# Kernel optimization log

Measured on AMD Instinct MI355X. Metric: run time of the kernel, lower is better.

## Reference

```python
import jax, jax.numpy as jnp
import numpy as np

B, S, V, E, H = 512, 512, 128, 128, 256


def setup_inputs() -> dict:
    key = jax.random.key(0)
    ks = jax.random.split(key, 12)
    s_e = 1.0 / np.sqrt(E)
    s_h = 1.0 / np.sqrt(H)
    inp = {
        "x": jax.random.randint(ks[0], (B, S), 0, V, dtype=jnp.int64),
        "emb": jax.random.normal(ks[1], (V, E), dtype=jnp.float32) * 0.02,
        # layer 0: input dim E
        "Wi0": jax.random.uniform(ks[2], (4 * H, E), jnp.float32, -s_e, s_e),
        "bi0": jax.random.uniform(ks[3], (4 * H,), jnp.float32, -s_e, s_e),
        "Wh0": jax.random.uniform(ks[4], (4 * H, H), jnp.float32, -s_h, s_h),
        "bh0": jax.random.uniform(ks[5], (4 * H,), jnp.float32, -s_h, s_h),
        # layer 1: input dim H
        "Wi1": jax.random.uniform(ks[6], (4 * H, H), jnp.float32, -s_h, s_h),
        "bi1": jax.random.uniform(ks[7], (4 * H,), jnp.float32, -s_h, s_h),
        "Wh1": jax.random.uniform(ks[8], (4 * H, H), jnp.float32, -s_h, s_h),
        "bh1": jax.random.uniform(ks[9], (4 * H,), jnp.float32, -s_h, s_h),
        # fc_gen: hidden -> vocab
        "Wg": jax.random.uniform(ks[10], (V, H), jnp.float32, -s_h, s_h),
        "bg": jax.random.uniform(ks[11], (V,), jnp.float32, -s_h, s_h),
    }
    return inp


def lstm_layer(x_seq, Wi, bi, Wh, bh):
    """x_seq: [B,S,D] -> hidden states [B,S,H]. Gate order f,i,g,o (chunk order)."""
    b, s, _ = x_seq.shape
    h_dim = Wh.shape[1]
    # precompute input contribution for all timesteps in one big matmul
    xg = jnp.einsum("bsd,gd->bsg", x_seq, Wi) + bi  # [B,S,4H]

    def step(carry, xg_t):
        h, c = carry
        gates = xg_t + h @ Wh.T + bh  # [B,4H]
        f, i, g, o = jnp.split(gates, 4, axis=-1)
        c = jax.nn.sigmoid(f) * c + jax.nn.sigmoid(i) * jnp.tanh(g)
        h = jax.nn.sigmoid(o) * jnp.tanh(c)
        return (h, c), h

    init = (jnp.zeros((b, h_dim), x_seq.dtype), jnp.zeros((b, h_dim), x_seq.dtype))
    _, hs = jax.lax.scan(step, init, jnp.swapaxes(xg, 0, 1))  # hs: [S,B,H]
    return jnp.swapaxes(hs, 0, 1)


def reference(x, emb, Wi0, bi0, Wh0, bh0, Wi1, bi1, Wh1, bh1, Wg, bg):
    # Embedding lookup
    e = emb[x]  # [B,S,E]
    # Forward-direction stacked LSTM (backward direction never affects logits;
    # dropout is identity at inference)
    h1 = lstm_layer(e, Wi0, bi0, Wh0, bh0)   # [B,S,H]
    h2 = lstm_layer(h1, Wi1, bi1, Wh1, bh1)  # [B,S,H]
    logits = h2 @ Wg.T + bg                  # [B,S,V]
    return logits
```

## Files before the change

kernel.cpp:

```cpp
#include <hip/hip_runtime.h>
#include <hip/hip_bf16.h>

#define BB 512
#define SS 512
#define EE 128
#define HH 256
#define VV 128
#define G4H 1024
#define TSL 64
#define NSEG (SS / TSL)

using bf16 = __bf16;
typedef __attribute__((ext_vector_type(8))) __bf16 bf16x8;
typedef __attribute__((ext_vector_type(4))) float f32x4;

__device__ __forceinline__ float rcpf(float x) { return __builtin_amdgcn_rcpf(x); }
__device__ __forceinline__ float exp2f_(float x) { return __builtin_amdgcn_exp2f(x); }
__device__ __forceinline__ float sigf(float x) {
  return rcpf(1.0f + exp2f_(-1.442695041f * x));
}
__device__ __forceinline__ float tanh_(float x) {
  return 2.0f * rcpf(1.0f + exp2f_(-2.885390082f * x)) - 1.0f;
}
__device__ __forceinline__ bf16x8 cvt8(const float* __restrict__ s) {
  bf16x8 f;
  #pragma unroll
  for (int j = 0; j < 8; ++j) f[j] = (bf16)s[j];
  return f;
}
__device__ __forceinline__ float bf2f(unsigned short u) {
  return __uint_as_float(((unsigned)u) << 16);
}

__global__ void detect_kernel(const int* __restrict__ x, int* __restrict__ flag) {
  const int i = blockIdx.x * 256 + threadIdx.x;
  if (x[2 * i + 1] != 0) atomicOr(flag, 1);
}

__global__ __launch_bounds__(256)
void table_kernel(const float* __restrict__ emb, const float* __restrict__ Wi,
                  const float* __restrict__ bi, const float* __restrict__ bh,
                  unsigned short* __restrict__ table) {
  const int g = blockIdx.x * 256 + threadIdx.x;
  const int v = blockIdx.y;
  float s = bi[g] + bh[g];
  const float* er = emb + v * EE;
  const float* wr = Wi + (size_t)g * EE;
  #pragma unroll 4
  for (int e = 0; e < EE; ++e) s += er[e] * wr[e];
  const bf16 b = (bf16)s;
  table[v * G4H + (g & 255) * 4 + (g >> 8)] = *(const unsigned short*)&b;
}

__global__ __launch_bounds__(256)
void wprep_kernel(const float* __restrict__ Wh0, const float* __restrict__ Wh1,
                  bf16x8* __restrict__ wb0, bf16x8* __restrict__ wb1) {
  const int idx = blockIdx.x * 256 + threadIdx.x;
  const int l = idx & 63, kc = (idx >> 6) & 7, s = (idx >> 9) & 7, w = idx >> 12;
  const int lg = l >> 4, ln = l & 15;
  const int n = (s >> 1) * HH + w * 32 + 16 * (s & 1) + ln;
  const int k0 = kc * 32 + lg * 8;
  const float* src = (blockIdx.y ? Wh1 : Wh0) + (size_t)n * HH + k0;
  (blockIdx.y ? wb1 : wb0)[idx] = cvt8(src);
}

__device__ __forceinline__
void rec0_body(char* smem, const int* __restrict__ x, int is32,
               const bf16x8* __restrict__ wb,
               const unsigned short* __restrict__ table,
               bf16* __restrict__ h1, float (*cst)[4],
               int t0, int bid, bool load_h) {
  bf16 (*hbuf)[4096] = (bf16(*)[4096])smem;
  bf16x8* wlds = (bf16x8*)(smem + 16384);
  const int tid = threadIdx.x, w = tid >> 6, l = tid & 63, lg = l >> 4, ln = l & 15;
  const int b0 = bid * 16, hb = w * 32;

  bf16x8 Wf[4][8];
  #pragma unroll
  for (int s = 0; s < 4; ++s)
    #pragma unroll
    for (int kc = 0; kc < 8; ++kc)
      Wf[s][kc] = wb[w * 4096 + s * 512 + kc * 64 + l];
  #pragma unroll
  for (int j = 0; j < 2; ++j)
    #pragma unroll
    for (int kc = 0; kc < 8; ++kc)
      wlds[((w * 2 + j) * 8 + kc) * 64 + l] = wb[w * 4096 + (6 + j) * 512 + kc * 64 + l];
  const bf16x8* __restrict__ gsrc0 = wb + w * 4096 + 4 * 512 + l;
  const bf16x8* __restrict__ gsrc1 = wb + w * 4096 + 5 * 512 + l;

  int hoff[4];
  #pragma unroll
  for (int r = 0; r < 4; ++r)
    hoff[r] = ((b0 + lg * 4 + r) * SS) * HH + hb + ln;

  if (t0 == 0) {
    bf16x8 z = {};
    ((bf16x8*)&hbuf[0][0])[tid] = z;
  } else if (load_h) {
    #pragma unroll
    for (int j = 0; j < 2; ++j)
      #pragma unroll
      for (int r = 0; r < 4; ++r) {
        const int m = lg * 4 + r, col = hb + 16 * j + ln;
        const bf16 hv = h1[((size_t)(b0 + m) * SS + (t0 - 1)) * HH + col];
        hbuf[0][(w * 64 + m * 4 + 2 * j + (ln >> 3)) * 8 + (ln & 7)] = hv;
      }
  }
  int idx[4];
  #pragma unroll
  for (int r = 0; r < 4; ++r) {
    const long xi = (long)(b0 + lg * 4 + r) * SS + t0;
    idx[r] = x[is32 ? xi : 2 * xi] & 127;
  }
  __syncthreads();

  #pragma unroll 1
  for (int tt = 0; tt < TSL; ++tt) {
    const int t = t0 + tt, p = tt & 1;
    ushort4 tj[4][2];
    #pragma unroll
    for (int r = 0; r < 4; ++r) {
      const unsigned short* base = table + (size_t)idx[r] * G4H + (hb + ln) * 4;
      tj[r][0] = *(const ushort4*)base;
      tj[r][1] = *(const ushort4*)(base + 64);
    }
    if (tt + 1 < TSL) {
      #pragma unroll
      for (int r = 0; r < 4; ++r) {
        const long xi = (long)(b0 + lg * 4 + r) * SS + (t + 1);
        idx[r] = x[is32 ? xi : 2 * xi] & 127;
      }
    }
    f32x4 acc[4][2] = {};
    #pragma unroll
    for (int kc = 0; kc < 8; ++kc) {
      bf16x8 a = ((const bf16x8*)&hbuf[p][0])[kc * 64 + ln * 4 + lg];
      acc[0][0] = __builtin_amdgcn_mfma_f32_16x16x32_bf16(a, Wf[0][kc], acc[0][0], 0, 0, 0);
      acc[0][1] = __builtin_amdgcn_mfma_f32_16x16x32_bf16(a, Wf[1][kc], acc[0][1], 0, 0, 0);
      acc[1][0] = __builtin_amdgcn_mfma_f32_16x16x32_bf16(a, Wf[2][kc], acc[1][0], 0, 0, 0);
      acc[1][1] = __builtin_amdgcn_mfma_f32_16x16x32_bf16(a, Wf[3][kc], acc[1][1], 0, 0, 0);
      acc[2][0] = __builtin_amdgcn_mfma_f32_16x16x32_bf16(a, gsrc0[kc * 64], acc[2][0], 0, 0, 0);
      acc[2][1] = __builtin_amdgcn_mfma_f32_16x16x32_bf16(a, gsrc1[kc * 64], acc[2][1], 0, 0, 0);
      #pragma unroll
      for (int j = 0; j < 2; ++j) {
        bf16x8 bw = wlds[((w * 2 + j) * 8 + kc) * 64 + l];
        acc[3][j] = __builtin_amdgcn_mfma_f32_16x16x32_bf16(a, bw, acc[3][j], 0, 0, 0);
      }
    }
    #pragma unroll
    for (int j = 0; j < 2; ++j)
      #pragma unroll
      for (int r = 0; r < 4; ++r) {
        const float fg = sigf(acc[0][j][r] + bf2f(tj[r][j].x));
        const float ig = sigf(acc[1][j][r] + bf2f(tj[r][j].y));
        const float gg = tanh_(acc[2][j][r] + bf2f(tj[r][j].z));
        const float og = sigf(acc[3][j][r] + bf2f(tj[r][j].w));
        const float cc = fg * cst[j][r] + ig * gg;
        cst[j][r] = cc;
        const bf16 hv = (bf16)(og * tanh_(cc));
        const int m = lg * 4 + r;
        hbuf[p ^ 1][(w * 64 + m * 4 + 2 * j + (ln >> 3)) * 8 + (ln & 7)] = hv;
        h1[hoff[r] + t * HH + 16 * j] = hv;
      }
    __syncthreads();
  }
}

__device__ __forceinline__
void rec1_body(char* smem, const unsigned short* __restrict__ xg,
               const bf16x8* __restrict__ wb, bf16* __restrict__ hreg,
               float* __restrict__ cws, int t0, int bid) {
  bf16 (*hbuf)[4096] = (bf16(*)[4096])smem;
  bf16x8* wlds = (bf16x8*)(smem + 16384);
  const int tid = threadIdx.x, w = tid >> 6, l = tid & 63, lg = l >> 4, ln = l & 15;
  const int b0 = bid * 16, hb = w * 32;

  bf16x8 Wf[4][8];
  #pragma unroll
  for (int s = 0; s < 4; ++s)
    #pragma unroll
    for (int kc = 0; kc < 8; ++kc)
      Wf[s][kc] = wb[w * 4096 + s * 512 + kc * 64 + l];
  #pragma unroll
  for (int j = 0; j < 2; ++j)
    #pragma unroll
    for (int kc = 0; kc < 8; ++kc)
      wlds[((w * 2 + j) * 8 + kc) * 64 + l] = wb[w * 4096 + (6 + j) * 512 + kc * 64 + l];
  const bf16x8* __restrict__ gsrc0 = wb + w * 4096 + 4 * 512 + l;
  const bf16x8* __restrict__ gsrc1 = wb + w * 4096 + 5 * 512 + l;

  int hoff[4];
  size_t xbase[4];
  #pragma unroll
  for (int r = 0; r < 4; ++r) {
    hoff[r] = ((b0 + lg * 4 + r) * SS) * HH + hb + ln;
    xbase[r] = (size_t)(b0 + lg * 4 + r) * TSL * G4H + (hb + ln) * 4;
  }

  float c[2][4];
  if (t0 == 0) {
    #pragma unroll
    for (int j = 0; j < 2; ++j)
      #pragma unroll
      for (int r = 0; r < 4; ++r) c[j][r] = 0.f;
    bf16x8 z = {};
    ((bf16x8*)&hbuf[0][0])[tid] = z;
  } else {
    #pragma unroll
    for (int j = 0; j < 2; ++j)
      #pragma unroll
      for (int r = 0; r < 4; ++r) {
        const int m = lg * 4 + r, col = hb + 16 * j + ln;
        c[j][r] = cws[(size_t)(b0 + m) * HH + col];
        const bf16 hv = hreg[((size_t)(b0 + m) * SS + (t0 - 1)) * HH + col];
        hbuf[0][(w * 64 + m * 4 + 2 * j + (ln >> 3)) * 8 + (ln & 7)] = hv;
      }
  }
  __syncthreads();

  #pragma unroll 1
  for (int tt = 0; tt < TSL; ++tt) {
    const int t = t0 + tt, p = tt & 1;
    ushort4 tj[4][2];
    #pragma unroll
    for (int r = 0; r < 4; ++r) {
      const unsigned short* base = xg + xbase[r] + (size_t)tt * G4H;
      tj[r][0] = *(const ushort4*)base;
      tj[r][1] = *(const ushort4*)(base + 64);
    }
    f32x4 acc[4][2] = {};
    #pragma unroll
    for (int kc = 0; kc < 8; ++kc) {
      bf16x8 a = ((const bf16x8*)&hbuf[p][0])[kc * 64 + ln * 4 + lg];
      acc[0][0] = __builtin_amdgcn_mfma_f32_16x16x32_bf16(a, Wf[0][kc], acc[0][0], 0, 0, 0);
      acc[0][1] = __builtin_amdgcn_mfma_f32_16x16x32_bf16(a, Wf[1][kc], acc[0][1], 0, 0, 0);
      acc[1][0] = __builtin_amdgcn_mfma_f32_16x16x32_bf16(a, Wf[2][kc], acc[1][0], 0, 0, 0);
      acc[1][1] = __builtin_amdgcn_mfma_f32_16x16x32_bf16(a, Wf[3][kc], acc[1][1], 0, 0, 0);
      acc[2][0] = __builtin_amdgcn_mfma_f32_16x16x32_bf16(a, gsrc0[kc * 64], acc[2][0], 0, 0, 0);
      acc[2][1] = __builtin_amdgcn_mfma_f32_16x16x32_bf16(a, gsrc1[kc * 64], acc[2][1], 0, 0, 0);
      #pragma unroll
      for (int j = 0; j < 2; ++j) {
        bf16x8 bw = wlds[((w * 2 + j) * 8 + kc) * 64 + l];
        acc[3][j] = __builtin_amdgcn_mfma_f32_16x16x32_bf16(a, bw, acc[3][j], 0, 0, 0);
      }
    }
    #pragma unroll
    for (int j = 0; j < 2; ++j)
      #pragma unroll
      for (int r = 0; r < 4; ++r) {
        const float fg = sigf(acc[0][j][r] + bf2f(tj[r][j].x));
        const float ig = sigf(acc[1][j][r] + bf2f(tj[r][j].y));
        const float gg = tanh_(acc[2][j][r] + bf2f(tj[r][j].z));
        const float og = sigf(acc[3][j][r] + bf2f(tj[r][j].w));
        const float cc = fg * c[j][r] + ig * gg;
        c[j][r] = cc;
        const bf16 hv = (bf16)(og * tanh_(cc));
        const int m = lg * 4 + r;
        hbuf[p ^ 1][(w * 64 + m * 4 + 2 * j + (ln >> 3)) * 8 + (ln & 7)] = hv;
        hreg[hoff[r] + t * HH + 16 * j] = hv;
      }
    __syncthreads();
  }
  #pragma unroll
  for (int j = 0; j < 2; ++j)
    #pragma unroll
    for (int r = 0; r < 4; ++r)
      cws[(size_t)(b0 + lg * 4 + r) * HH + hb + 16 * j + ln] = c[j][r];
}

__device__ __forceinline__
void xg_body(char* smem, const bf16* __restrict__ A, const float* __restrict__ W,
             const float* __restrict__ bias0, const float* __restrict__ bias1,
             bf16* __restrict__ out, int t0, int flat) {
  bf16x8* alds = (bf16x8*)smem;
  bf16x8* blds = (bf16x8*)(smem + 65536);
  const int tid = threadIdx.x, w = tid >> 6, l = tid & 63, lg = l >> 4, ln = l & 15;
  const int wm = w & 1, wn = w >> 1;
  const int R0 = (flat & 255) * 128, N0 = (flat >> 8) * 128;
  {
    const int row = tid >> 2, seg = tid & 3;
    const int R = R0 + row;
    const bf16* asrc = A + ((size_t)(R >> 6) * SS + t0 + (R & 63)) * HH + seg * 64;
    #pragma unroll
    for (int k = 0; k < 8; ++k) {
      const int g = seg * 8 + k;
      alds[row * 32 + (g ^ (row & 7))] = *(const bf16x8*)(asrc + k * 8);
    }
    const float* bsrc = W + (size_t)(N0 + row) * HH + seg * 64;
    #pragma unroll
    for (int k = 0; k < 8; ++k) {
      const int g = seg * 8 + k;
      blds[row * 32 + (g ^ (row & 7))] = cvt8(bsrc + k * 8);
    }
  }
  __syncthreads();
  f32x4 acc[4][2] = {};
  #pragma unroll
  for (int kc = 0; kc < 8; ++kc) {
    bf16x8 bfr[2];
    #pragma unroll
    for (int nt = 0; nt < 2; ++nt) {
      const int row = wn * 32 + nt * 16 + ln;
      bfr[nt] = blds[row * 32 + ((kc * 4 + lg) ^ (row & 7))];
    }
    #pragma unroll
    for (int mt = 0; mt < 4; ++mt) {
      const int row = wm * 64 + mt * 16 + ln;
      bf16x8 a = alds[row * 32 + ((kc * 4 + lg) ^ (row & 7))];
      #pragma unroll
      for (int nt = 0; nt < 2; ++nt)
        acc[mt][nt] = __builtin_amdgcn_mfma_f32_16x16x32_bf16(a, bfr[nt], acc[mt][nt], 0, 0, 0);
    }
  }
  #pragma unroll
  for (int nt = 0; nt < 2; ++nt) {
    const int n = N0 + wn * 32 + nt * 16 + ln;
    const float bv = bias0[n] + bias1[n];
    const int col = (n & 255) * 4 + (n >> 8);
    #pragma unroll
    for (int mt = 0; mt < 4; ++mt)
      #pragma unroll
      for (int r = 0; r < 4; ++r) {
        const size_t row = (size_t)R0 + wm * 64 + mt * 16 + lg * 4 + r;
        out[row * G4H + col] = (bf16)(acc[mt][nt][r] + bv);
      }
  }
}

__device__ __forceinline__
void rec0_slice(char* smem, const int* x, int is32, const bf16x8* wb0,
                const unsigned short* table, bf16* hreg, float* cws0,
                int t0, int bid) {
  const int tid = threadIdx.x, w = tid >> 6, l = tid & 63, lg = l >> 4, ln = l & 15;
  const int b0 = bid * 16, hb = w * 32;
  float c[2][4];
  if (t0 == 0) {
    #pragma unroll
    for (int j = 0; j < 2; ++j)
      #pragma unroll
      for (int r = 0; r < 4; ++r) c[j][r] = 0.f;
  } else {
    #pragma unroll
    for (int j = 0; j < 2; ++j)
      #pragma unroll
      for (int r = 0; r < 4; ++r)
        c[j][r] = cws0[(size_t)(b0 + lg * 4 + r) * HH + hb + 16 * j + ln];
  }
  rec0_body(smem, x, is32, wb0, table, hreg, c, t0, bid, t0 != 0);
  #pragma unroll
  for (int j = 0; j < 2; ++j)
    #pragma unroll
    for (int r = 0; r < 4; ++r)
      cws0[(size_t)(b0 + lg * 4 + r) * HH + hb + 16 * j + ln] = c[j][r];
}

__global__ __launch_bounds__(512)
void pipe_kernel(const int* __restrict__ x, const int* __restrict__ flagp,
                 const bf16x8* __restrict__ wb0,
                 const unsigned short* __restrict__ table,
                 const unsigned short* __restrict__ xg_in,
                 const bf16x8* __restrict__ wb1,
                 bf16* __restrict__ hreg, float* __restrict__ cws0,
                 float* __restrict__ cws1, int k,
                 const float* __restrict__ Wi, const float* __restrict__ bi,
                 const float* __restrict__ bh, bf16* __restrict__ xg_out) {
  __shared__ __align__(16) char smem[147456];
  const int bx = blockIdx.x;
  if (bx < 32) {
    if (k < NSEG) rec0_slice(smem, x, *flagp, wb0, table, hreg, cws0, k * TSL, bx);
  } else if (bx < 64) {
    if (k >= 2) rec1_body(smem, xg_in, wb1, hreg, cws1, (k - 2) * TSL, bx - 32);
  } else {
    if (k >= 1 && k <= NSEG)
      xg_body(smem, hreg, Wi, bi, bh, xg_out, (k - 1) * TSL, bx - 64);
  }
}

__global__ __launch_bounds__(512)
void rec0_full_kernel(const int* __restrict__ x, const int* __restrict__ flagp,
                      const bf16x8* __restrict__ wb,
                      const unsigned short* __restrict__ table,
                      bf16* __restrict__ h1) {
  __shared__ __align__(16) char smem[147456];
  const int is32 = *flagp;
  float c[2][4] = {};
  #pragma unroll 1
  for (int s = 0; s < NSEG; ++s) {
    rec0_body(smem, x, is32, wb, table, h1, c, s * TSL, blockIdx.x, false);
    __syncthreads();
  }
}

__global__ __launch_bounds__(512)
void combo_kernel(const unsigned short* __restrict__ xg_in,
                  const bf16x8* __restrict__ wb, bf16* __restrict__ hreg,
                  float* __restrict__ cws, int t0,
                  const float* __restrict__ Wi, const float* __restrict__ bi,
                  const float* __restrict__ bh, bf16* __restrict__ xg_out) {
  __shared__ __align__(16) char smem[147456];
  if (blockIdx.x < 32)
    rec1_body(smem, xg_in, wb, hreg, cws, t0, blockIdx.x);
  else
    xg_body(smem, hreg, Wi, bi, bh, xg_out, t0 + TSL, blockIdx.x - 32);
}

template <int OUT_BF16>
__global__ __launch_bounds__(512)
void gemm_kernel(const bf16* __restrict__ A, const float* __restrict__ W,
                 const float* __restrict__ bias0, const float* __restrict__ bias1,
                 void* __restrict__ out, int t0, int NCOL) {
  __shared__ bf16x8 alds[4096];
  __shared__ bf16x8 blds[4096];
  const int tid = threadIdx.x, w = tid >> 6, l = tid & 63, lg = l >> 4, ln = l & 15;
  const int wm = w & 1, wn = w >> 1;
  const int R0 = blockIdx.x * 128, N0 = blockIdx.y * 128;
  {
    const int row = tid >> 2, seg = tid & 3;
    const bf16* asrc;
    if (OUT_BF16) {
      const int R = R0 + row;
      asrc = A + ((size_t)(R >> 6) * SS + t0 + (R & 63)) * HH + seg * 64;
    } else {
      asrc = A + ((size_t)R0 + row) * HH + seg * 64;
    }
    #pragma unroll
    for (int k = 0; k < 8; ++k) {
      const int g = seg * 8 + k;
      alds[row * 32 + (g ^ (row & 7))] = *(const bf16x8*)(asrc + k * 8);
    }
    const float* bsrc = W + (size_t)(N0 + row) * HH + seg * 64;
    #pragma unroll
    for (int k = 0; k < 8; ++k) {
      const int g = seg * 8 + k;
      blds[row * 32 + (g ^ (row & 7))] = cvt8(bsrc + k * 8);
    }
  }
  __syncthreads();
  f32x4 acc[4][2] = {};
  #pragma unroll
  for (int kc = 0; kc < 8; ++kc) {
    bf16x8 bfr[2];
    #pragma unroll
    for (int nt = 0; nt < 2; ++nt) {
      const int row = wn * 32 + nt * 16 + ln;
      bfr[nt] = blds[row * 32 + ((kc * 4 + lg) ^ (row & 7))];
    }
    #pragma unroll
    for (int mt = 0; mt < 4; ++mt) {
      const int row = wm * 64 + mt * 16 + ln;
      bf16x8 a = alds[row * 32 + ((kc * 4 + lg) ^ (row & 7))];
      #pragma unroll
      for (int nt = 0; nt < 2; ++nt)
        acc[mt][nt] = __builtin_amdgcn_mfma_f32_16x16x32_bf16(a, bfr[nt], acc[mt][nt], 0, 0, 0);
    }
  }
  #pragma unroll
  for (int nt = 0; nt < 2; ++nt) {
    const int n = N0 + wn * 32 + nt * 16 + ln;
    const float bv = bias0[n] + (bias1 ? bias1[n] : 0.f);
    const int col = OUT_BF16 ? ((n & 255) * 4 + (n >> 8)) : n;
    #pragma unroll
    for (int mt = 0; mt < 4; ++mt)
      #pragma unroll
      for (int r = 0; r < 4; ++r) {
        const size_t row = (size_t)R0 + wm * 64 + mt * 16 + lg * 4 + r;
        if (OUT_BF16) ((bf16*)out)[row * NCOL + col] = (bf16)(acc[mt][nt][r] + bv);
        else          ((float*)out)[row * NCOL + col] = acc[mt][nt][r] + bv;
      }
  }
}

extern "C" void kernel_launch(void* const* d_in, const int* in_sizes, int n_in,
                              void* d_out, int out_size, void* d_ws, size_t ws_size,
                              hipStream_t stream) {
  const int*   x   = (const int*)d_in[0];
  const float* emb = (const float*)d_in[1];
  const float* Wi0 = (const float*)d_in[2];
  const float* bi0 = (const float*)d_in[3];
  const float* Wh0 = (const float*)d_in[4];
  const float* bh0 = (const float*)d_in[5];
  const float* Wi1 = (const float*)d_in[6];
  const float* bi1 = (const float*)d_in[7];
  const float* Wh1 = (const float*)d_in[8];
  const float* bh1 = (const float*)d_in[9];
  const float* Wg  = (const float*)d_in[10];
  const float* bg  = (const float*)d_in[11];

  char* ws = (char*)d_ws;
  int* flag = (int*)ws;
  unsigned short* table = (unsigned short*)(ws + 256);
  bf16x8* wb0 = (bf16x8*)(ws + 256 + 262144);
  bf16x8* wb1 = (bf16x8*)(ws + 256 + 262144 + 524288);
  bf16* hreg = (bf16*)(ws + 256 + 262144 + 524288 + 524288);
  const size_t need_base = 256 + 262144 + 524288 + 524288
                         + (size_t)BB * SS * HH * sizeof(bf16);
  float* cws0 = (float*)(ws + need_base);
  float* cws1 = (float*)(ws + need_base + 524288);
  const size_t need_full = need_base + 2 * 524288;
  if (ws_size < need_base) return;

  bf16* xgbuf0 = (bf16*)d_out;
  bf16* xgbuf1 = (bf16*)((char*)d_out + (size_t)BB * TSL * G4H * sizeof(bf16));

  (void)hipMemsetAsync(flag, 0, sizeof(int), stream);
  detect_kernel<<<dim3(8), dim3(256), 0, stream>>>(x, flag);
  table_kernel<<<dim3(4, 128), dim3(256), 0, stream>>>(emb, Wi0, bi0, bh0, table);
  wprep_kernel<<<dim3(128, 2), dim3(256), 0, stream>>>(Wh0, Wh1, wb0, wb1);

  if (ws_size >= need_full) {
    for (int k = 0; k <= NSEG + 1; ++k) {
      bf16* xin  = (k & 1) ? xgbuf1 : xgbuf0;
      bf16* xout = (k & 1) ? xgbuf0 : xgbuf1;
      const bool xgv = (k >= 1 && k <= NSEG);
      const int nblk = 64 + (xgv ? 2048 : 0);
      pipe_kernel<<<dim3(nblk), dim3(512), 0, stream>>>(
          x, flag, wb0, table, (const unsigned short*)xin, wb1,
          hreg, cws0, cws1, k, Wi1, bi1, bh1, xout);
    }
  } else {
    float* cwsA = (float*)wb0;
    rec0_full_kernel<<<dim3(32), dim3(512), 0, stream>>>(x, flag, wb0, table, hreg);
    gemm_kernel<1><<<dim3(256, 8), dim3(512), 0, stream>>>(
        hreg, Wi1, bi1, bh1, xgbuf0, 0, G4H);
    for (int s = 0; s < NSEG; ++s) {
      const int t0 = s * TSL;
      bf16* xin  = (s & 1) ? xgbuf1 : xgbuf0;
      bf16* xout = (s & 1) ? xgbuf0 : xgbuf1;
      const int nblk = 32 + ((s + 1 < NSEG) ? 2048 : 0);
      combo_kernel<<<dim3(nblk), dim3(512), 0, stream>>>(
          (const unsigned short*)xin, wb1, hreg, cwsA, t0, Wi1, bi1, bh1, xout);
    }
  }
  gemm_kernel<0><<<dim3(BB * SS / 128, VV / 128), dim3(512), 0, stream>>>(
      hreg, Wg, bg, nullptr, d_out, 0, VV);
}
```

Baseline: 2.882 ms.

## Retile layer-1 input-gate GEMM to 64x256 tiles with gate-interleaved weight columns

The xg GEMM tile changes from 128 rows x 128 columns to 64 rows (one batch row block across 64 timesteps) x 256 interleaved gate columns. Weight rows are gathered so the output columns come out contiguous in the interleaved gate layout. This is meant to give each tile contiguous row reads and coalesced, contiguous output writes. The cost is a larger B tile, so each 64-row A tile is paired with four times more weight conversion work, and LDS grows to 160KB. The generic gemm template is split into separate xg and projection kernels.

```diff
diff --git a/kernel.cpp b/kernel.cpp
--- a/kernel.cpp
+++ b/kernel.cpp
@@ -274,56 +274,59 @@
              const float* __restrict__ bias0, const float* __restrict__ bias1,
              bf16* __restrict__ out, int t0, int flat) {
   bf16x8* alds = (bf16x8*)smem;
-  bf16x8* blds = (bf16x8*)(smem + 65536);
+  bf16x8* blds = (bf16x8*)(smem + 32768);
   const int tid = threadIdx.x, w = tid >> 6, l = tid & 63, lg = l >> 4, ln = l & 15;
   const int wm = w & 1, wn = w >> 1;
-  const int R0 = (flat & 255) * 128, N0 = (flat >> 8) * 128;
+  const int rb = flat & 511, up = flat >> 9;
+  const int R0 = rb * 64;
   {
-    const int row = tid >> 2, seg = tid & 3;
-    const int R = R0 + row;
-    const bf16* asrc = A + ((size_t)(R >> 6) * SS + t0 + (R & 63)) * HH + seg * 64;
-    #pragma unroll
-    for (int k = 0; k < 8; ++k) {
-      const int g = seg * 8 + k;
+    const int row = tid >> 3, seg = tid & 7;
+    const bf16* asrc = A + ((size_t)rb * SS + t0 + row) * HH + seg * 32;
+    #pragma unroll
+    for (int k = 0; k < 4; ++k) {
+      const int g = seg * 4 + k;
       alds[row * 32 + (g ^ (row & 7))] = *(const bf16x8*)(asrc + k * 8);
     }
-    const float* bsrc = W + (size_t)(N0 + row) * HH + seg * 64;
-    #pragma unroll
-    for (int k = 0; k < 8; ++k) {
-      const int g = seg * 8 + k;
-      blds[row * 32 + (g ^ (row & 7))] = cvt8(bsrc + k * 8);
+    const int col = tid >> 1, half = tid & 1;
+    const int n = (col & 3) * HH + up * 64 + (col >> 2);
+    const float* bsrc = W + (size_t)n * HH + half * 128;
+    #pragma unroll
+    for (int k = 0; k < 16; ++k) {
+      const int g = half * 16 + k;
+      blds[col * 32 + (g ^ (col & 7))] = cvt8(bsrc + k * 8);
     }
   }
   __syncthreads();
-  f32x4 acc[4][2] = {};
+  f32x4 acc[2][4] = {};
   #pragma unroll
   for (int kc = 0; kc < 8; ++kc) {
-    bf16x8 bfr[2];
-    #pragma unroll
-    for (int nt = 0; nt < 2; ++nt) {
-      const int row = wn * 32 + nt * 16 + ln;
+    bf16x8 bfr[4];
+    #pragma unroll
+    for (int nt = 0; nt < 4; ++nt) {
+      const int row = wn * 64 + nt * 16 + ln;
       bfr[nt] = blds[row * 32 + ((kc * 4 + lg) ^ (row & 7))];
     }
     #pragma unroll
-    for (int mt = 0; mt < 4; ++mt) {
-      const int row = wm * 64 + mt * 16 + ln;
+    for (int mt = 0; mt < 2; ++mt) {
+      const int row = wm * 32 + mt * 16 + ln;
       bf16x8 a = alds[row * 32 + ((kc * 4 + lg) ^ (row & 7))];
       #pragma unroll
-      for (int nt = 0; nt < 2; ++nt)
+      for (int nt = 0; nt < 4; ++nt)
         acc[mt][nt] = __builtin_amdgcn_mfma_f32_16x16x32_bf16(a, bfr[nt], acc[mt][nt], 0, 0, 0);
     }
   }
   #pragma unroll
-  for (int nt = 0; nt < 2; ++nt) {
-    const int n = N0 + wn * 32 + nt * 16 + ln;
+  for (int nt = 0; nt < 4; ++nt) {
+    const int local = wn * 64 + nt * 16 + ln;
+    const int n = (local & 3) * HH + up * 64 + (local >> 2);
     const float bv = bias0[n] + bias1[n];
-    const int col = (n & 255) * 4 + (n >> 8);
-    #pragma unroll
-    for (int mt = 0; mt < 4; ++mt)
-      #pragma unroll
-      for (int r = 0; r < 4; ++r) {
-        const size_t row = (size_t)R0 + wm * 64 + mt * 16 + lg * 4 + r;
-        out[row * G4H + col] = (bf16)(acc[mt][nt][r] + bv);
+    const int gcol = up * 256 + local;
+    #pragma unroll
+    for (int mt = 0; mt < 2; ++mt)
+      #pragma unroll
+      for (int r = 0; r < 4; ++r) {
+        const size_t row = (size_t)R0 + wm * 32 + mt * 16 + lg * 4 + r;
+        out[row * G4H + gcol] = (bf16)(acc[mt][nt][r] + bv);
       }
   }
 }
@@ -365,7 +368,7 @@
                  float* __restrict__ cws1, int k,
                  const float* __restrict__ Wi, const float* __restrict__ bi,
                  const float* __restrict__ bh, bf16* __restrict__ xg_out) {
-  __shared__ __align__(16) char smem[147456];
+  __shared__ __align__(16) char smem[163840];
   const int bx = blockIdx.x;
   if (bx < 32) {
     if (k < NSEG) rec0_slice(smem, x, *flagp, wb0, table, hreg, cws0, k * TSL, bx);
@@ -398,18 +401,24 @@
                   float* __restrict__ cws, int t0,
                   const float* __restrict__ Wi, const float* __restrict__ bi,
                   const float* __restrict__ bh, bf16* __restrict__ xg_out) {
-  __shared__ __align__(16) char smem[147456];
+  __shared__ __align__(16) char smem[163840];
   if (blockIdx.x < 32)
     rec1_body(smem, xg_in, wb, hreg, cws, t0, blockIdx.x);
   else
     xg_body(smem, hreg, Wi, bi, bh, xg_out, t0 + TSL, blockIdx.x - 32);
 }
 
-template <int OUT_BF16>
 __global__ __launch_bounds__(512)
-void gemm_kernel(const bf16* __restrict__ A, const float* __restrict__ W,
-                 const float* __restrict__ bias0, const float* __restrict__ bias1,
-                 void* __restrict__ out, int t0, int NCOL) {
+void xg_kernel(const bf16* __restrict__ A, const float* __restrict__ W,
+               const float* __restrict__ bi, const float* __restrict__ bh,
+               bf16* __restrict__ out, int t0) {
+  __shared__ __align__(16) char smem[163840];
+  xg_body(smem, A, W, bi, bh, out, t0, blockIdx.x);
+}
+
+__global__ __launch_bounds__(512)
+void proj_kernel(const bf16* __restrict__ A, const float* __restrict__ W,
+                 const float* __restrict__ bias0, float* __restrict__ out) {
   __shared__ bf16x8 alds[4096];
   __shared__ bf16x8 blds[4096];
   const int tid = threadIdx.x, w = tid >> 6, l = tid & 63, lg = l >> 4, ln = l & 15;
@@ -417,13 +426,7 @@
   const int R0 = blockIdx.x * 128, N0 = blockIdx.y * 128;
   {
     const int row = tid >> 2, seg = tid & 3;
-    const bf16* asrc;
-    if (OUT_BF16) {
-      const int R = R0 + row;
-      asrc = A + ((size_t)(R >> 6) * SS + t0 + (R & 63)) * HH + seg * 64;
-    } else {
-      asrc = A + ((size_t)R0 + row) * HH + seg * 64;
-    }
+    const bf16* asrc = A + ((size_t)R0 + row) * HH + seg * 64;
     #pragma unroll
     for (int k = 0; k < 8; ++k) {
       const int g = seg * 8 + k;
@@ -458,15 +461,13 @@
   #pragma unroll
   for (int nt = 0; nt < 2; ++nt) {
     const int n = N0 + wn * 32 + nt * 16 + ln;
-    const float bv = bias0[n] + (bias1 ? bias1[n] : 0.f);
-    const int col = OUT_BF16 ? ((n & 255) * 4 + (n >> 8)) : n;
+    const float bv = bias0[n];
     #pragma unroll
     for (int mt = 0; mt < 4; ++mt)
       #pragma unroll
       for (int r = 0; r < 4; ++r) {
         const size_t row = (size_t)R0 + wm * 64 + mt * 16 + lg * 4 + r;
-        if (OUT_BF16) ((bf16*)out)[row * NCOL + col] = (bf16)(acc[mt][nt][r] + bv);
-        else          ((float*)out)[row * NCOL + col] = acc[mt][nt][r] + bv;
+        out[row * VV + n] = acc[mt][nt][r] + bv;
       }
   }
 }
@@ -521,8 +522,7 @@
   } else {
     float* cwsA = (float*)wb0;
     rec0_full_kernel<<<dim3(32), dim3(512), 0, stream>>>(x, flag, wb0, table, hreg);
-    gemm_kernel<1><<<dim3(256, 8), dim3(512), 0, stream>>>(
-        hreg, Wi1, bi1, bh1, xgbuf0, 0, G4H);
+    xg_kernel<<<dim3(2048), dim3(512), 0, stream>>>(hreg, Wi1, bi1, bh1, xgbuf0, 0);
     for (int s = 0; s < NSEG; ++s) {
       const int t0 = s * TSL;
       bf16* xin  = (s & 1) ? xgbuf1 : xgbuf0;
@@ -532,6 +532,6 @@
           (const unsigned short*)xin, wb1, hreg, cwsA, t0, Wi1, bi1, bh1, xout);
     }
   }
-  gemm_kernel<0><<<dim3(BB * SS / 128, VV / 128), dim3(512), 0, stream>>>(
-      hreg, Wg, bg, nullptr, d_out, 0, VV);
-}
+  proj_kernel<<<dim3(BB * SS / 128, VV / 128), dim3(512), 0, stream>>>(
+      hreg, Wg, bg, (float*)d_out);
+}
```

New measurement: 2.713 ms. -5.9%, faster.
